# Kernel optimization log

Measured on AMD Instinct MI355X. Metric: run time of the kernel, lower is better.

## Reference

```python
import jax, jax.numpy as jnp
import numpy as np

B, C, N, H, W = 8, 128, 16, 56, 56
HID, OUT = 128, 128


def conv1x1(x, w, b):
    # 1x1x1 Conv3d == channel-mixing GEMM. x: [B,Cin,N,H,W], w: [Cout,Cin], b: [Cout]
    return jnp.einsum('oc,bcnhw->bonhw', w, x) + b[None, :, None, None, None]


def setup_inputs() -> dict:
    key = jax.random.key(0)
    ks = jax.random.split(key, 9)
    s = 0.02
    return {
        'x': jax.random.normal(ks[0], (B, C, N, H, W), dtype=jnp.float32),
        'w_q': jax.random.normal(ks[1], (HID, C), dtype=jnp.float32) * s,
        'b_q': jax.random.normal(ks[2], (HID,), dtype=jnp.float32) * s,
        'w_k': jax.random.normal(ks[3], (HID, C), dtype=jnp.float32) * s,
        'b_k': jax.random.normal(ks[4], (HID,), dtype=jnp.float32) * s,
        'w_v': jax.random.normal(ks[5], (HID, C), dtype=jnp.float32) * s,
        'b_v': jax.random.normal(ks[6], (HID,), dtype=jnp.float32) * s,
        'w_o': jax.random.normal(ks[7], (OUT, HID), dtype=jnp.float32) * s,
        'b_o': jax.random.normal(ks[8], (OUT,), dtype=jnp.float32) * s,
    }


def reference(x, w_q, b_q, w_k, b_k, w_v, b_v, w_o, b_o):
    Bsz, Cc, Nn, Hh, Ww = x.shape
    L = Nn * Hh * Ww
    q = conv1x1(x, w_q, b_q).reshape(Bsz, -1, L)   # [B, hid, L]
    k = conv1x1(x, w_k, b_k).reshape(Bsz, -1, L)   # [B, hid, L]
    v = conv1x1(x, w_v, b_v).reshape(Bsz, -1, L)   # [B, hid, L]
    # NOTE: attention is over CHANNELS (hid x hid), since k was transposed to [B, L, hid]
    attn = jax.nn.softmax(jnp.einsum('bql,bkl->bqk', q, k), axis=-1)  # [B, hid, hid]
    feats = jnp.einsum('bqk,bkl->bql', attn, v).reshape(Bsz, -1, Nn, Hh, Ww)
    out = conv1x1(feats, w_o, b_o) + x             # residual requires out_dim == in_dim
    return jnp.mean(out, axis=2)                   # mean over N (depth) -> [B, out, H, W]
```

## Files before the change

kernel.cpp:

```cpp
#include <hip/hip_runtime.h>
#include <hip/hip_bf16.h>
#include <cstdint>

#define BB   8
#define CCH  128
#define NND  16
#define HWD  3136
#define LLT  50176
#define HWB  32
#define NHB  98
#define K3WB 64
#define K3NB 49

#define OFF_SP  0
#define OFF_RP  12845056
#define OFF_S   12945408
#define OFF_M   13076480
#define OFF_Q   13207552
#define OFF_AV  13338624
#define OFF_CV  13339648

typedef __attribute__((ext_vector_type(8)))  short bf16x8;
typedef __attribute__((ext_vector_type(16))) float f32x16;

__device__ __forceinline__ uint32_t fbits(float f){ union{float f;uint32_t u;}v; v.f=f; return v.u; }
__device__ __forceinline__ float bitsf(uint32_t u){ union{uint32_t u;float f;}v; v.u=u; return v.f; }

#define MFMA32(a,b,c) __builtin_amdgcn_mfma_f32_32x32x16_bf16((a),(b),(c),0,0,0)

__global__ __launch_bounds__(256,4) void k1_gram(const float* __restrict__ x,
    float* __restrict__ Sp, float* __restrict__ rp, float* __restrict__ Y)
{
  __shared__ __align__(16) short lds_h[2][4*129*8];
  __shared__ __align__(16) short lds_l[2][4*129*8];
  const int b   = blockIdx.x / NHB;
  const int hb  = blockIdx.x % NHB;
  const int hw0 = hb * HWB;
  const int tid = threadIdx.x;
  const int lane = tid & 63, w = tid >> 6;
  const int wr = w >> 1, wc = w & 1;
  const int cr = tid >> 3;
  const int p  = tid & 7;
  const int kc = p >> 1, hf = p & 1;
  const float* xb = x + (size_t)b*CCH*LLT + (size_t)cr*LLT + hw0 + 4*p;

  f32x16 acc[2][2];
  #pragma unroll
  for(int ai=0;ai<2;ai++)
    #pragma unroll
    for(int bi=0;bi<2;bi++)
      #pragma unroll
      for(int e=0;e<16;e++) acc[ai][bi][e] = 0.f;
  float yac[16];
  #pragma unroll
  for(int i=0;i<16;i++) yac[i]=0.f;

  float4 v[4];
  #pragma unroll
  for(int j=0;j<4;j++) v[j] = *(const float4*)(xb + (size_t)(32*j)*LLT);

#define SPLIT(bufi)                                                         \
  {                                                                         \
    _Pragma("unroll")                                                       \
    for(int j=0;j<4;j++){                                                   \
      const int c = 32*j + cr;                                              \
      const float x0=v[j].x, x1=v[j].y, x2=v[j].z, x3=v[j].w;               \
      const uint32_t a0=fbits(x0),a1=fbits(x1),a2=fbits(x2),a3=fbits(x3);   \
      const int h0 = __builtin_amdgcn_perm(a1, a0, 0x07060302u);            \
      const int h1 = __builtin_amdgcn_perm(a3, a2, 0x07060302u);            \
      const float l0 = x0 - bitsf(a0&0xFFFF0000u);                          \
      const float l1 = x1 - bitsf(a1&0xFFFF0000u);                          \
      const float l2 = x2 - bitsf(a2&0xFFFF0000u);                          \
      const float l3 = x3 - bitsf(a3&0xFFFF0000u);                          \
      const int g0 = __builtin_amdgcn_perm(fbits(l1), fbits(l0), 0x07060302u); \
      const int g1 = __builtin_amdgcn_perm(fbits(l3), fbits(l2), 0x07060302u); \
      const int sa = (kc*129 + c)*8 + 4*hf;                                 \
      *(int2*)&lds_h[bufi][sa] = make_int2(h0,h1);                          \
      *(int2*)&lds_l[bufi][sa] = make_int2(g0,g1);                          \
      yac[4*j+0]+=x0; yac[4*j+1]+=x1; yac[4*j+2]+=x2; yac[4*j+3]+=x3;       \
    }                                                                       \
  }

  SPLIT(0);
  __syncthreads();
  #pragma unroll
  for(int j=0;j<4;j++) v[j] = *(const float4*)(xb + (size_t)(32*j)*LLT + HWD);

  for(int n=0;n<NND;n++){
    const int cur = n & 1;
    #pragma unroll
    for(int ks=0;ks<2;ks++){
      const int kk = 2*ks + (lane>>5);
      const int rbase = (kk*129 + (lane&31))*8;
      const bf16x8 a0h = *(const bf16x8*)&lds_h[cur][rbase + (64*wr    )*8];
      const bf16x8 a0l = *(const bf16x8*)&lds_l[cur][rbase + (64*wr    )*8];
      const bf16x8 a1h = *(const bf16x8*)&lds_h[cur][rbase + (64*wr+32)*8];
      const bf16x8 a1l = *(const bf16x8*)&lds_l[cur][rbase + (64*wr+32)*8];
      const bf16x8 b0h = *(const bf16x8*)&lds_h[cur][rbase + (64*wc    )*8];
      const bf16x8 b0l = *(const bf16x8*)&lds_l[cur][rbase + (64*wc    )*8];
      const bf16x8 b1h = *(const bf16x8*)&lds_h[cur][rbase + (64*wc+32)*8];
      const bf16x8 b1l = *(const bf16x8*)&lds_l[cur][rbase + (64*wc+32)*8];
      acc[0][0] = MFMA32(a0h, b0h, acc[0][0]);
      acc[0][0] = MFMA32(a0h, b0l, acc[0][0]);
      acc[0][0] = MFMA32(a0l, b0h, acc[0][0]);
      acc[0][1] = MFMA32(a0h, b1h, acc[0][1]);
      acc[0][1] = MFMA32(a0h, b1l, acc[0][1]);
      acc[0][1] = MFMA32(a0l, b1h, acc[0][1]);
      acc[1][0] = MFMA32(a1h, b0h, acc[1][0]);
      acc[1][0] = MFMA32(a1h, b0l, acc[1][0]);
      acc[1][0] = MFMA32(a1l, b0h, acc[1][0]);
      acc[1][1] = MFMA32(a1h, b1h, acc[1][1]);
      acc[1][1] = MFMA32(a1h, b1l, acc[1][1]);
      acc[1][1] = MFMA32(a1l, b1h, acc[1][1]);
    }
    if(n+1 < NND){
      SPLIT(cur^1);
      __syncthreads();
      if(n+2 < NND){
        #pragma unroll
        for(int j=0;j<4;j++)
          v[j] = *(const float4*)(xb + (size_t)(32*j)*LLT + (size_t)(n+2)*HWD);
      }
    }
  }
#undef SPLIT

  #pragma unroll
  for(int j=0;j<4;j++){
    float4 o4 = make_float4(yac[4*j]*0.0625f, yac[4*j+1]*0.0625f,
                            yac[4*j+2]*0.0625f, yac[4*j+3]*0.0625f);
    *(float4*)(Y + ((size_t)b*CCH + 32*j + cr)*HWD + hw0 + 4*p) = o4;
  }
  #pragma unroll
  for(int j=0;j<4;j++){
    float s = yac[4*j]+yac[4*j+1]+yac[4*j+2]+yac[4*j+3];
    #pragma unroll
    for(int st=1;st<8;st<<=1) s += __shfl_xor(s, st, 8);
    if(p==0) rp[(size_t)(b*NHB+hb)*CCH + 32*j + cr] = s;
  }

  float* Sb = Sp + (size_t)(b*NHB+hb)*CCH*CCH;
  const int col = lane & 31, roff = 4*(lane>>5);
  #pragma unroll
  for(int ai=0;ai<2;ai++)
    #pragma unroll
    for(int bi=0;bi<2;bi++)
      #pragma unroll
      for(int reg=0;reg<16;reg++){
        const int row = 64*wr + 32*ai + roff + (reg&3) + 8*(reg>>2);
        Sb[(size_t)row*CCH + 64*wc + 32*bi + col] = acc[ai][bi][reg];
      }
}

__global__ __launch_bounds__(256) void k1r(const float* __restrict__ Sp,
                                           float* __restrict__ S)
{
  const int b  = blockIdx.x >> 4;
  const int ch = blockIdx.x & 15;
  const int i  = ch*1024 + threadIdx.x*4;
  const float* p = Sp + (size_t)b*NHB*CCH*CCH + i;
  float4 s = make_float4(0.f,0.f,0.f,0.f);
  for(int hb=0;hb<NHB;hb++){
    float4 v = *(const float4*)(p + (size_t)hb*CCH*CCH);
    s.x+=v.x; s.y+=v.y; s.z+=v.z; s.w+=v.w;
  }
  *(float4*)(S + (size_t)b*CCH*CCH + i) = s;
}

__global__ __launch_bounds__(256) void k2ab(const float* __restrict__ S, const float* __restrict__ rp,
    const float* __restrict__ wq, const float* __restrict__ bq,
    const float* __restrict__ wk, const float* __restrict__ bk,
    const float* __restrict__ wv, const float* __restrict__ bv,
    float* __restrict__ M, float* __restrict__ av)
{
  __shared__ __align__(16) float t1[16][132];
  __shared__ float rb_s[CCH];
  __shared__ float wrk_s[CCH];
  __shared__ float wrq_s[16];
  const int b   = blockIdx.x >> 3;
  const int r0  = (blockIdx.x & 7) * 16;
  const int tid = threadIdx.x;
  const float* Sb = S + (size_t)b*CCH*CCH;

  if(tid < CCH){
    float s = 0.f;
    const float* rpb = rp + (size_t)b*NHB*CCH + tid;
    for(int hb=0;hb<NHB;hb++) s += rpb[hb*CCH];
    rb_s[tid] = s;
  }
  __syncthreads();

  if(tid < CCH){
    float s = 0.f;
    for(int m=0;m<CCH;m++) s += wk[(size_t)tid*CCH+m]*rb_s[m];
    wrk_s[tid] = s;
  } else if(tid < CCH+16){
    const int rr2 = tid - CCH;
    float s = 0.f;
    for(int m=0;m<CCH;m++) s += wq[(size_t)(r0+rr2)*CCH+m]*rb_s[m];
    wrq_s[rr2] = s;
  }

  const int rr = tid >> 4;
  const int c0 = (tid & 15) * 8;
  {
    float a8[8] = {0,0,0,0,0,0,0,0};
    const float* wqr = wq + (size_t)(r0+rr)*CCH;
    for(int m4=0;m4<32;m4++){
      float4 w4 = *(const float4*)(wqr + 4*m4);
      const float wl[4] = {w4.x,w4.y,w4.z,w4.w};
      #pragma unroll
      for(int mm=0;mm<4;mm++){
        const int m = 4*m4+mm;
        const float w = wl[mm];
        float4 s0 = *(const float4*)(Sb + (size_t)m*CCH + c0);
        float4 s1 = *(const float4*)(Sb + (size_t)m*CCH + c0 + 4);
        a8[0]=fmaf(w,s0.x,a8[0]); a8[1]=fmaf(w,s0.y,a8[1]);
        a8[2]=fmaf(w,s0.z,a8[2]); a8[3]=fmaf(w,s0.w,a8[3]);
        a8[4]=fmaf(w,s1.x,a8[4]); a8[5]=fmaf(w,s1.y,a8[5]);
        a8[6]=fmaf(w,s1.z,a8[6]); a8[7]=fmaf(w,s1.w,a8[7]);
      }
    }
    #pragma unroll
    for(int j=0;j<8;j++) t1[rr][c0+j] = a8[j];
  }
  __syncthreads();

  const int j0 = c0;
  float g[8] = {0,0,0,0,0,0,0,0};
  for(int c4=0;c4<32;c4++){
    float4 tv = *(const float4*)(&t1[rr][4*c4]);
    #pragma unroll
    for(int jj=0;jj<8;jj++){
      float4 w4 = *(const float4*)(wk + (size_t)(j0+jj)*CCH + 4*c4);
      g[jj]=fmaf(tv.x,w4.x,g[jj]); g[jj]=fmaf(tv.y,w4.y,g[jj]);
      g[jj]=fmaf(tv.z,w4.z,g[jj]); g[jj]=fmaf(tv.w,w4.w,g[jj]);
    }
  }
  const float bqr  = bq[r0+rr];
  const float wrqr = wrq_s[rr];
  #pragma unroll
  for(int jj=0;jj<8;jj++)
    g[jj] += wrqr*bk[j0+jj] + bqr*wrk_s[j0+jj] + (float)LLT*bqr*bk[j0+jj];

  float mx = g[0];
  #pragma unroll
  for(int jj=1;jj<8;jj++) mx = fmaxf(mx, g[jj]);
  #pragma unroll
  for(int s=1;s<16;s<<=1) mx = fmaxf(mx, __shfl_xor(mx, s, 16));
  float ex[8], sum=0.f;
  #pragma unroll
  for(int jj=0;jj<8;jj++){ ex[jj] = expf(g[jj]-mx); sum += ex[jj]; }
  #pragma unroll
  for(int s=1;s<16;s<<=1) sum += __shfl_xor(sum, s, 16);
  const float inv = 1.0f/sum;

  float pa = 0.f;
  #pragma unroll
  for(int jj=0;jj<8;jj++) pa += ex[jj]*inv*bv[j0+jj];
  #pragma unroll
  for(int s=1;s<16;s<<=1) pa += __shfl_xor(pa, s, 16);
  if((tid&15)==0) av[b*CCH + r0+rr] = pa;

  __syncthreads();
  #pragma unroll
  for(int jj=0;jj<8;jj++) t1[rr][j0+jj] = ex[jj]*inv;
  __syncthreads();

  {
    float a8[8] = {0,0,0,0,0,0,0,0};
    for(int k4=0;k4<32;k4++){
      float4 a4 = *(const float4*)(&t1[rr][4*k4]);
      const float al[4] = {a4.x,a4.y,a4.z,a4.w};
      #pragma unroll
      for(int kk=0;kk<4;kk++){
        const int k = 4*k4+kk;
        const float wgt = al[kk];
        float4 v0 = *(const float4*)(wv + (size_t)k*CCH + c0);
        float4 v1 = *(const float4*)(wv + (size_t)k*CCH + c0 + 4);
        a8[0]=fmaf(wgt,v0.x,a8[0]); a8[1]=fmaf(wgt,v0.y,a8[1]);
        a8[2]=fmaf(wgt,v0.z,a8[2]); a8[3]=fmaf(wgt,v0.w,a8[3]);
        a8[4]=fmaf(wgt,v1.x,a8[4]); a8[5]=fmaf(wgt,v1.y,a8[5]);
        a8[6]=fmaf(wgt,v1.z,a8[6]); a8[7]=fmaf(wgt,v1.w,a8[7]);
      }
    }
    float* Mr = M + ((size_t)b*CCH + r0+rr)*CCH + c0;
    *(float4*)(Mr  ) = make_float4(a8[0],a8[1],a8[2],a8[3]);
    *(float4*)(Mr+4) = make_float4(a8[4],a8[5],a8[6],a8[7]);
  }
}

__global__ __launch_bounds__(256) void k2c(const float* __restrict__ M,
    const float* __restrict__ wo, const float* __restrict__ bo,
    const float* __restrict__ av, float* __restrict__ Q, float* __restrict__ cv)
{
  const int b  = blockIdx.x >> 3;
  const int o0 = (blockIdx.x & 7)*16;
  const int tid = threadIdx.x;
  const int rr = tid>>4, c0 = (tid&15)*8;
  const int o  = o0 + rr;
  const float* wor = wo + (size_t)o*CCH;
  const float* Mb  = M + (size_t)b*CCH*CCH;
  float a8[8] = {0,0,0,0,0,0,0,0};
  for(int m4=0;m4<32;m4++){
    float4 w4 = *(const float4*)(wor + 4*m4);
    const float wl[4] = {w4.x,w4.y,w4.z,w4.w};
    #pragma unroll
    for(int mm=0;mm<4;mm++){
      const int m = 4*m4+mm;
      const float w = wl[mm];
      float4 v0 = *(const float4*)(Mb + (size_t)m*CCH + c0);
      float4 v1 = *(const float4*)(Mb + (size_t)m*CCH + c0 + 4);
      a8[0]=fmaf(w,v0.x,a8[0]); a8[1]=fmaf(w,v0.y,a8[1]);
      a8[2]=fmaf(w,v0.z,a8[2]); a8[3]=fmaf(w,v0.w,a8[3]);
      a8[4]=fmaf(w,v1.x,a8[4]); a8[5]=fmaf(w,v1.y,a8[5]);
      a8[6]=fmaf(w,v1.z,a8[6]); a8[7]=fmaf(w,v1.w,a8[7]);
    }
  }
  #pragma unroll
  for(int j=0;j<8;j++) if(o == c0+j) a8[j] += 1.0f;
  float* Qr = Q + ((size_t)b*CCH + o)*CCH + c0;
  *(float4*)(Qr  ) = make_float4(a8[0],a8[1],a8[2],a8[3]);
  *(float4*)(Qr+4) = make_float4(a8[4],a8[5],a8[6],a8[7]);

  if(tid < 16){
    const int oo = o0 + tid;
    float s = 0.f;
    for(int m=0;m<CCH;m++) s += wo[(size_t)oo*CCH+m]*av[b*CCH+m];
    cv[b*CCH + oo] = s + bo[oo];
  }
}

__global__ __launch_bounds__(256,2) void k3(const float* __restrict__ Q,
    const float* __restrict__ cv, float* __restrict__ out)
{
  __shared__ __align__(16) float4 qs[4096];
  const int b   = blockIdx.x / K3NB;
  const int hb  = blockIdx.x % K3NB;
  const int hw0 = hb * K3WB;
  const int tid = threadIdx.x;

  const float4* Qg = (const float4*)(Q + (size_t)b*CCH*CCH);
  #pragma unroll
  for(int it=0; it<16; it++){
    const int idx = it*256 + tid;
    const int row = idx >> 5, ch = idx & 31;
    qs[(row<<5) | (ch ^ (row>>3))] = Qg[idx];
  }
  __syncthreads();

  const int tx = tid & 15, ty = tid >> 4;
  const int o0 = tx*8;
  const int hg = ty*4;
  float acc[8][4];
  #pragma unroll
  for(int i=0;i<8;i++){ acc[i][0]=0.f; acc[i][1]=0.f; acc[i][2]=0.f; acc[i][3]=0.f; }

  const float* Yb = out + (size_t)b*CCH*HWD + hw0 + hg;
  for(int c4=0;c4<32;c4++){
    float4 yv[4];
    #pragma unroll
    for(int mm=0;mm<4;mm++) yv[mm] = *(const float4*)(Yb + (size_t)(4*c4+mm)*HWD);
    #pragma unroll
    for(int i=0;i<8;i++){
      const int row = o0 + i;
      const float4 q4 = qs[(row<<5) | (c4 ^ tx)];
      const float ql[4] = {q4.x,q4.y,q4.z,q4.w};
      #pragma unroll
      for(int mm=0;mm<4;mm++){
        acc[i][0]=fmaf(ql[mm],yv[mm].x,acc[i][0]);
        acc[i][1]=fmaf(ql[mm],yv[mm].y,acc[i][1]);
        acc[i][2]=fmaf(ql[mm],yv[mm].z,acc[i][2]);
        acc[i][3]=fmaf(ql[mm],yv[mm].w,acc[i][3]);
      }
    }
  }
  __syncthreads();
  #pragma unroll
  for(int i=0;i<8;i++){
    const float c = cv[b*CCH + o0+i];
    float4 o4 = make_float4(acc[i][0]+c, acc[i][1]+c, acc[i][2]+c, acc[i][3]+c);
    *(float4*)(out + ((size_t)b*CCH + o0+i)*HWD + hw0 + hg) = o4;
  }
}

extern "C" void kernel_launch(void* const* d_in, const int* in_sizes, int n_in,
                              void* d_out, int out_size, void* d_ws, size_t ws_size,
                              hipStream_t stream) {
  const float* x  = (const float*)d_in[0];
  const float* wq = (const float*)d_in[1];
  const float* bq = (const float*)d_in[2];
  const float* wk = (const float*)d_in[3];
  const float* bk = (const float*)d_in[4];
  const float* wv = (const float*)d_in[5];
  const float* bv = (const float*)d_in[6];
  const float* wo = (const float*)d_in[7];
  const float* bo = (const float*)d_in[8];
  float* out = (float*)d_out;
  float* ws  = (float*)d_ws;

  k1_gram<<<BB*NHB, 256, 0, stream>>>(x, ws+OFF_SP, ws+OFF_RP, out);
  k1r<<<128, 256, 0, stream>>>(ws+OFF_SP, ws+OFF_S);
  k2ab<<<64, 256, 0, stream>>>(ws+OFF_S, ws+OFF_RP, wq, bq, wk, bk, wv, bv,
                               ws+OFF_M, ws+OFF_AV);
  k2c<<<64, 256, 0, stream>>>(ws+OFF_M, wo, bo, ws+OFF_AV, ws+OFF_Q, ws+OFF_CV);
  k3<<<BB*K3NB, 256, 0, stream>>>(ws+OFF_Q, ws+OFF_CV, out);
}
```

Measured before the change: 165.5 us.

## Reduce Gram partials via atomics into 8 slices and store depth-mean as bf16

Each k1_gram block previously wrote a full 128x128 partial Gram matrix (98 per batch), which k1r then read back and summed. Blocks now atomically add into one of 8 slices per batch, and row sums are atomically accumulated directly. This cuts the partial-buffer traffic and the reduction pass, at the cost of a new zeroing kernel, atomic contention, and nondeterministic summation order. The depth-mean intermediate Y is also stored as bf16 in the workspace instead of fp32 in the output buffer, halving k3's input reads but adding rounding error to the residual path.

```diff
diff --git a/kernel.cpp b/kernel.cpp
--- a/kernel.cpp
+++ b/kernel.cpp
@@ -12,24 +12,38 @@
 #define K3WB 64
 #define K3NB 49
 
-#define OFF_SP  0
-#define OFF_RP  12845056
-#define OFF_S   12945408
-#define OFF_M   13076480
-#define OFF_Q   13207552
-#define OFF_AV  13338624
-#define OFF_CV  13339648
+#define OFF_S8  0
+#define OFF_R   1048576
+#define OFF_S   1049600
+#define OFF_M   1180672
+#define OFF_Q   1311744
+#define OFF_AV  1442816
+#define OFF_CV  1443840
+#define OFF_YB  1444864
+#define ZEROFL  1049600
 
 typedef __attribute__((ext_vector_type(8)))  short bf16x8;
 typedef __attribute__((ext_vector_type(16))) float f32x16;
 
 __device__ __forceinline__ uint32_t fbits(float f){ union{float f;uint32_t u;}v; v.f=f; return v.u; }
 __device__ __forceinline__ float bitsf(uint32_t u){ union{uint32_t u;float f;}v; v.u=u; return v.f; }
+__device__ __forceinline__ float bf2f(unsigned short u){ return bitsf(((uint32_t)u)<<16); }
+__device__ __forceinline__ unsigned short f2bf_rne(float f){
+  uint32_t u = fbits(f);
+  u += 0x7FFFu + ((u>>16)&1u);
+  return (unsigned short)(u>>16);
+}
 
 #define MFMA32(a,b,c) __builtin_amdgcn_mfma_f32_32x32x16_bf16((a),(b),(c),0,0,0)
 
-__global__ __launch_bounds__(256,4) void k1_gram(const float* __restrict__ x,
-    float* __restrict__ Sp, float* __restrict__ rp, float* __restrict__ Y)
+__global__ __launch_bounds__(256) void zk(float* __restrict__ w)
+{
+  const int i = (blockIdx.x*256 + threadIdx.x)*4;
+  if(i < ZEROFL) *(float4*)(w + i) = make_float4(0.f,0.f,0.f,0.f);
+}
+
+__global__ __launch_bounds__(256,3) void k1_gram(const float* __restrict__ x,
+    float* __restrict__ S8, float* __restrict__ r, unsigned short* __restrict__ Yb)
 {
   __shared__ __align__(16) short lds_h[2][4*129*8];
   __shared__ __align__(16) short lds_l[2][4*129*8];
@@ -127,19 +141,22 @@
 
   #pragma unroll
   for(int j=0;j<4;j++){
-    float4 o4 = make_float4(yac[4*j]*0.0625f, yac[4*j+1]*0.0625f,
-                            yac[4*j+2]*0.0625f, yac[4*j+3]*0.0625f);
-    *(float4*)(Y + ((size_t)b*CCH + 32*j + cr)*HWD + hw0 + 4*p) = o4;
+    ushort4 o4;
+    o4.x = f2bf_rne(yac[4*j+0]*0.0625f);
+    o4.y = f2bf_rne(yac[4*j+1]*0.0625f);
+    o4.z = f2bf_rne(yac[4*j+2]*0.0625f);
+    o4.w = f2bf_rne(yac[4*j+3]*0.0625f);
+    *(ushort4*)(Yb + ((size_t)b*CCH + 32*j + cr)*HWD + hw0 + 4*p) = o4;
   }
   #pragma unroll
   for(int j=0;j<4;j++){
     float s = yac[4*j]+yac[4*j+1]+yac[4*j+2]+yac[4*j+3];
     #pragma unroll
     for(int st=1;st<8;st<<=1) s += __shfl_xor(s, st, 8);
-    if(p==0) rp[(size_t)(b*NHB+hb)*CCH + 32*j + cr] = s;
-  }
-
-  float* Sb = Sp + (size_t)(b*NHB+hb)*CCH*CCH;
+    if(p==0) atomicAdd(&r[b*CCH + 32*j + cr], s);
+  }
+
+  float* Sb = S8 + (size_t)(b*8 + (blockIdx.x & 7))*CCH*CCH;
   const int col = lane & 31, roff = 4*(lane>>5);
   #pragma unroll
   for(int ai=0;ai<2;ai++)
@@ -148,26 +165,26 @@
       #pragma unroll
       for(int reg=0;reg<16;reg++){
         const int row = 64*wr + 32*ai + roff + (reg&3) + 8*(reg>>2);
-        Sb[(size_t)row*CCH + 64*wc + 32*bi + col] = acc[ai][bi][reg];
+        atomicAdd(&Sb[(size_t)row*CCH + 64*wc + 32*bi + col], acc[ai][bi][reg]);
       }
 }
 
-__global__ __launch_bounds__(256) void k1r(const float* __restrict__ Sp,
-                                           float* __restrict__ S)
-{
-  const int b  = blockIdx.x >> 4;
-  const int ch = blockIdx.x & 15;
-  const int i  = ch*1024 + threadIdx.x*4;
-  const float* p = Sp + (size_t)b*NHB*CCH*CCH + i;
+__global__ __launch_bounds__(256) void k1r8(const float* __restrict__ S8,
+                                            float* __restrict__ S)
+{
+  const int b = blockIdx.x >> 4;
+  const int i = (blockIdx.x & 15)*1024 + threadIdx.x*4;
+  const float* p = S8 + (size_t)b*8*CCH*CCH + i;
   float4 s = make_float4(0.f,0.f,0.f,0.f);
-  for(int hb=0;hb<NHB;hb++){
-    float4 v = *(const float4*)(p + (size_t)hb*CCH*CCH);
+  #pragma unroll
+  for(int sl=0;sl<8;sl++){
+    float4 v = *(const float4*)(p + (size_t)sl*CCH*CCH);
     s.x+=v.x; s.y+=v.y; s.z+=v.z; s.w+=v.w;
   }
   *(float4*)(S + (size_t)b*CCH*CCH + i) = s;
 }
 
-__global__ __launch_bounds__(256) void k2ab(const float* __restrict__ S, const float* __restrict__ rp,
+__global__ __launch_bounds__(256) void k2ab(const float* __restrict__ S, const float* __restrict__ r,
     const float* __restrict__ wq, const float* __restrict__ bq,
     const float* __restrict__ wk, const float* __restrict__ bk,
     const float* __restrict__ wv, const float* __restrict__ bv,
@@ -182,12 +199,7 @@
   const int tid = threadIdx.x;
   const float* Sb = S + (size_t)b*CCH*CCH;
 
-  if(tid < CCH){
-    float s = 0.f;
-    const float* rpb = rp + (size_t)b*NHB*CCH + tid;
-    for(int hb=0;hb<NHB;hb++) s += rpb[hb*CCH];
-    rb_s[tid] = s;
-  }
+  if(tid < CCH) rb_s[tid] = r[b*CCH + tid];
   __syncthreads();
 
   if(tid < CCH){
@@ -332,7 +344,8 @@
 }
 
 __global__ __launch_bounds__(256,2) void k3(const float* __restrict__ Q,
-    const float* __restrict__ cv, float* __restrict__ out)
+    const float* __restrict__ cv, const unsigned short* __restrict__ Ybf,
+    float* __restrict__ out)
 {
   __shared__ __align__(16) float4 qs[4096];
   const int b   = blockIdx.x / K3NB;
@@ -356,11 +369,14 @@
   #pragma unroll
   for(int i=0;i<8;i++){ acc[i][0]=0.f; acc[i][1]=0.f; acc[i][2]=0.f; acc[i][3]=0.f; }
 
-  const float* Yb = out + (size_t)b*CCH*HWD + hw0 + hg;
+  const unsigned short* Ybb = Ybf + (size_t)b*CCH*HWD + hw0 + hg;
   for(int c4=0;c4<32;c4++){
     float4 yv[4];
     #pragma unroll
-    for(int mm=0;mm<4;mm++) yv[mm] = *(const float4*)(Yb + (size_t)(4*c4+mm)*HWD);
+    for(int mm=0;mm<4;mm++){
+      ushort4 u = *(const ushort4*)(Ybb + (size_t)(4*c4+mm)*HWD);
+      yv[mm] = make_float4(bf2f(u.x), bf2f(u.y), bf2f(u.z), bf2f(u.w));
+    }
     #pragma unroll
     for(int i=0;i<8;i++){
       const int row = o0 + i;
@@ -375,7 +391,6 @@
       }
     }
   }
-  __syncthreads();
   #pragma unroll
   for(int i=0;i<8;i++){
     const float c = cv[b*CCH + o0+i];
@@ -398,11 +413,13 @@
   const float* bo = (const float*)d_in[8];
   float* out = (float*)d_out;
   float* ws  = (float*)d_ws;
-
-  k1_gram<<<BB*NHB, 256, 0, stream>>>(x, ws+OFF_SP, ws+OFF_RP, out);
-  k1r<<<128, 256, 0, stream>>>(ws+OFF_SP, ws+OFF_S);
-  k2ab<<<64, 256, 0, stream>>>(ws+OFF_S, ws+OFF_RP, wq, bq, wk, bk, wv, bv,
-                               ws+OFF_M, ws+OFF_AV);
-  k2c<<<64, 256, 0, stream>>>(ws+OFF_M, wo, bo, ws+OFF_AV, ws+OFF_Q, ws+OFF_CV);
-  k3<<<BB*K3NB, 256, 0, stream>>>(ws+OFF_Q, ws+OFF_CV, out);
-}
+  unsigned short* ybf = (unsigned short*)(ws + OFF_YB);
+
+  zk     <<<1025, 256, 0, stream>>>(ws + OFF_S8);
+  k1_gram<<<BB*NHB, 256, 0, stream>>>(x, ws+OFF_S8, ws+OFF_R, ybf);
+  k1r8   <<<128, 256, 0, stream>>>(ws+OFF_S8, ws+OFF_S);
+  k2ab   <<<64, 256, 0, stream>>>(ws+OFF_S, ws+OFF_R, wq, bq, wk, bk, wv, bv,
+                                  ws+OFF_M, ws+OFF_AV);
+  k2c    <<<64, 256, 0, stream>>>(ws+OFF_M, wo, bo, ws+OFF_AV, ws+OFF_Q, ws+OFF_CV);
+  k3     <<<BB*K3NB, 256, 0, stream>>>(ws+OFF_Q, ws+OFF_CV, ybf, out);
+}
```

New measurement: 187.6 us. +13.3%, slower.
